# Kernel optimization log

Measured on AMD Instinct MI355X. Metric: run time of the kernel, lower is better.

## Reference

```python
import jax, jax.numpy as jnp
from jax import lax
import numpy as np

NSTART, NOPEN, NHID, NCLOSE, NLAYERS, KSZ, N = 40, 128, 256, 3, 40, 9, 1024
H_STEP = 0.1
PAD = (KSZ - 1) // 2  # 4 -> same-length conv
EPS = 1e-5


def conv1(x, K):
    # x: (1, Cin, N), K: (Cout, Cin, k); cross-correlation like torch F.conv1d
    return lax.conv_general_dilated(x, K, (1,), [(PAD, PAD)],
                                    dimension_numbers=('NCH', 'OIH', 'NCH'))


def conv1T(x, K):
    # torch F.conv_transpose1d(x, K, padding=PAD) == conv1d with swapped-channel,
    # flipped kernel and padding k-1-PAD (= PAD here since k=9, PAD=4)
    Kt = jnp.flip(jnp.swapaxes(K, 0, 1), -1)
    return lax.conv_general_dilated(x, Kt, (1,), [(PAD, PAD)],
                                    dimension_numbers=('NCH', 'OIH', 'NCH'))


def instance_norm(x):
    # x: (1, C, N); normalize per channel over spatial dim, biased var, no affine
    m = jnp.mean(x, axis=-1, keepdims=True)
    v = jnp.var(x, axis=-1, keepdims=True)
    return (x - m) * lax.rsqrt(v + EPS)


def get_graph_lap(Z):
    # Z: (C, N). Normalized Gaussian-affinity graph Laplacian.
    sq = jnp.sum(Z * Z, axis=0)  # (N,)
    D2 = jnp.maximum(sq[:, None] + sq[None, :] - 2.0 * (Z.T @ Z), 0.0)
    sigma = jnp.mean(D2) + 1e-12
    Wg = jnp.exp(-D2 / sigma)
    deg = jnp.sum(Wg, axis=1)
    Dh = lax.rsqrt(deg)
    L = Dh[:, None] * (jnp.diag(deg) - Wg) * Dh[None, :]
    return L, deg


def double_sym_layer(Z, Wi, Bi, L):
    # Z: (nopen, N), Wi: (2, nhid, nopen, 9), Bi: (2, nopen, 1), L: (N, N)
    A0 = instance_norm(conv1((Z + Bi[0])[None], Wi[0]))
    A1 = instance_norm((conv1((Z + Bi[1])[None], Wi[1])[0] @ L)[None])
    A0 = jax.nn.relu(A0)
    A1 = jax.nn.relu(A1)
    A0 = conv1T(A0, Wi[0])[0]
    A1 = conv1T(A1, Wi[1])[0] @ L.T
    return A0 + A1  # (nopen, N)


def setup_inputs() -> dict:
    key = jax.random.key(0)
    k1, k2, k3, k4, k5 = jax.random.split(key, 5)
    Z = jax.random.normal(k1, (NSTART, N), dtype=jnp.float32)
    stdv_o = 0.001 * NOPEN / NSTART
    Kopen = jax.random.uniform(k2, (NOPEN, NSTART), minval=-stdv_o, maxval=stdv_o, dtype=jnp.float32)
    stdv_c = 0.001 * NCLOSE / NOPEN
    Kclose = jax.random.uniform(k3, (NCLOSE, NOPEN), minval=-stdv_c, maxval=stdv_c, dtype=jnp.float32)
    W = jax.random.uniform(k4, (NLAYERS, 2, NHID, NOPEN, KSZ), minval=-1e-4, maxval=1e-4, dtype=jnp.float32)
    Bias = jax.random.uniform(k5, (NLAYERS, 2, NOPEN, 1), dtype=jnp.float32) * 1e-4
    return {"Z": Z, "Kopen": Kopen, "Kclose": Kclose, "W": W, "Bias": Bias}


def reference(Z, Kopen, Kclose, W, Bias):
    h = H_STEP
    Zc = Kopen @ Z          # (nopen, N)
    Zold = Zc
    L, _ = get_graph_lap(Zc)
    for i in range(NLAYERS):
        if i % 10 == 0:
            L, _ = get_graph_lap(Zc)
        Ai = double_sym_layer(Zc, W[i], Bias[i], L)
        Zc, Zold = 2.0 * Zc - Zold - (h * h) * Ai, Zc  # leapfrog step
    return (Kclose @ Zc, Kclose @ Zold)
```

## Files before the change

kernel.cpp:

```cpp
#include <hip/hip_runtime.h>

#define NN 1024
#define NOPEN 128
#define NHID 256
#define NSTART 40
#define NCLOSE 3
#define NLAYERS 40
#define KSZ 9

static constexpr float H2 = 0.01f;
static constexpr float IN_EPS = 1e-5f;

using floatx4 = __attribute__((ext_vector_type(4))) float;
using bfrag = __attribute__((ext_vector_type(8))) short;

__device__ __forceinline__ ushort f2bf(float f) {
    union { float f; unsigned u; } v; v.f = f;
    unsigned r = v.u + 0x7fffu + ((v.u >> 16) & 1u);
    return (ushort)(r >> 16);
}

__device__ __forceinline__ void prepw_piece(const float* __restrict__ W, ushort* __restrict__ Wf1,
                                            ushort* __restrict__ Wf2, int lb, int lsrc, int tid) {
    if (lb < 72) {
        int z = lb / 36, rem = lb % 36;
        int t = rem >> 2, q = rem & 3;
        const float* Wz = W + (size_t)(lsrc * 2 + z) * (NHID * NOPEN * KSZ);
        ushort* dst = Wf1 + (((size_t)(z * 9 + t) * 64 + q * 16) << 9);
#pragma unroll
        for (int r = 0; r < 32; ++r) {
            int ei = r * 256 + tid;
            int g = q * 4 + (ei >> 11);
            int kc = (ei >> 9) & 3;
            int lm = (ei >> 3) & 15, lq = (ei >> 7) & 3;
            int e = ei & 7;
            int co = g * 16 + lm, ci = kc * 32 + lq * 8 + e;
            dst[ei] = f2bf(Wz[co * (NOPEN * KSZ) + ci * KSZ + t]);
        }
    } else {
        int p2 = lb - 72;
        int z = p2 / 36, rem = p2 % 36;
        int t = rem >> 2, q = rem & 3;
        const float* Wz = W + (size_t)(lsrc * 2 + z) * (NHID * NOPEN * KSZ);
        ushort* dst = Wf2 + (((size_t)(z * 9 + t) * 64 + q * 16) << 9);
#pragma unroll
        for (int r = 0; r < 32; ++r) {
            int ei = r * 256 + tid;
            int fb = q * 16 + (ei >> 9);
            int g = fb >> 3, j = fb & 7;
            int lm = (ei >> 3) & 15, lq = (ei >> 7) & 3;
            int e = ei & 7;
            int ci = g * 16 + lm, co = j * 32 + lq * 8 + e;
            dst[ei] = f2bf(Wz[co * (NOPEN * KSZ) + ci * KSZ + t]);
        }
    }
}

__global__ __launch_bounds__(256) void k_open(const float* __restrict__ Kopen, const float* __restrict__ Z,
                       float* __restrict__ Zc, float* __restrict__ Zold,
                       const float* __restrict__ Bias0, ushort* __restrict__ Zct,
                       ushort* __restrict__ At0, ushort* __restrict__ At1,
                       const float* __restrict__ W, ushort* __restrict__ Wf1,
                       ushort* __restrict__ Wf2, float* __restrict__ sig, float* __restrict__ A1) {
    const int v = blockIdx.x, tid = threadIdx.x;
    if (v < 512) {
        int o = v >> 2, n = (v & 3) * 256 + tid;
        float acc = 0.f;
#pragma unroll
        for (int s = 0; s < NSTART; ++s)
            acc = fmaf(Kopen[o * NSTART + s], Z[s * NN + n], acc);
        Zc[o * NN + n] = acc;
        Zold[o * NN + n] = acc;
#pragma unroll
        for (int z = 0; z < 2; ++z)
            Zct[z * (1032 * 128) + (n + 4) * 128 + o] = f2bf(acc + Bias0[z * NOPEN + o]);
    } else if (v < 656) {
        prepw_piece(W, Wf1, Wf2, v - 512, 0, tid);
    } else if (v == 656) {
        if (tid == 0) sig[0] = 0.f;
        for (int idx = tid; idx < 1024; idx += 256) {
            int z = idx >> 9, rr = idx & 511;
            ushort* Zz = Zct + z * (1032 * 128);
            Zz[rr] = 0; Zz[1028 * 128 + rr] = 0;
        }
        for (int idx = tid; idx < 2048; idx += 256) {
            int a = idx >> 10, rr = idx & 1023;
            ushort* A = a ? At1 : At0;
            A[rr] = 0; A[1028 * 256 + rr] = 0;
        }
    } else {
        int b = v - 657;
        size_t base = (size_t)b * 4096 + tid * 4;
        float4 z4 = {0.f, 0.f, 0.f, 0.f};
#pragma unroll
        for (int r = 0; r < 4; ++r) *(float4*)&A1[base + r * 1024] = z4;
    }
}

__global__ __launch_bounds__(256) void k_d2(const float* __restrict__ Zc,
                                            float* __restrict__ D2, float* __restrict__ sig) {
    __shared__ __align__(16) float Zi[32 * 36];
    __shared__ __align__(16) float Zj[32 * 68];
    __shared__ float sqi[32], sqj[64];
    __shared__ float red[4];
    const int tid = threadIdx.x;
    const int tx = tid & 15, ty = tid >> 4;
    const int j0 = blockIdx.x * 64, i0 = blockIdx.y * 32;
    if (tid < 32) sqi[tid] = 0.f;
    else if (tid < 96) sqj[tid - 32] = 0.f;
    float acc[2][4] = {};
    for (int c0 = 0; c0 < NOPEN; c0 += 32) {
        for (int idx = tid; idx < 32 * 32; idx += 256) {
            int c = idx >> 5, ii = idx & 31;
            Zi[c * 36 + ii] = Zc[(c0 + c) * NN + i0 + ii];
        }
        for (int idx = tid; idx < 32 * 64; idx += 256) {
            int c = idx >> 6, jj = idx & 63;
            Zj[c * 68 + jj] = Zc[(c0 + c) * NN + j0 + jj];
        }
        __syncthreads();
        if (tid < 32) {
            float s = 0.f;
            for (int c = 0; c < 32; ++c) { float x = Zi[c * 36 + tid]; s = fmaf(x, x, s); }
            sqi[tid] += s;
        } else if (tid < 96) {
            int jj = tid - 32;
            float s = 0.f;
            for (int c = 0; c < 32; ++c) { float x = Zj[c * 68 + jj]; s = fmaf(x, x, s); }
            sqj[jj] += s;
        }
#pragma unroll 8
        for (int c = 0; c < 32; ++c) {
            float2 zi = *(const float2*)&Zi[c * 36 + ty * 2];
            float4 zj = *(const float4*)&Zj[c * 68 + tx * 4];
            acc[0][0] = fmaf(zi.x, zj.x, acc[0][0]);
            acc[0][1] = fmaf(zi.x, zj.y, acc[0][1]);
            acc[0][2] = fmaf(zi.x, zj.z, acc[0][2]);
            acc[0][3] = fmaf(zi.x, zj.w, acc[0][3]);
            acc[1][0] = fmaf(zi.y, zj.x, acc[1][0]);
            acc[1][1] = fmaf(zi.y, zj.y, acc[1][1]);
            acc[1][2] = fmaf(zi.y, zj.z, acc[1][2]);
            acc[1][3] = fmaf(zi.y, zj.w, acc[1][3]);
        }
        __syncthreads();
    }
    float part = 0.f;
#pragma unroll
    for (int m = 0; m < 2; ++m) {
        int i = i0 + ty * 2 + m;
        float sqi_v = sqi[ty * 2 + m];
        float4 d;
        d.x = fmaxf(sqi_v + sqj[tx * 4 + 0] - 2.f * acc[m][0], 0.f);
        d.y = fmaxf(sqi_v + sqj[tx * 4 + 1] - 2.f * acc[m][1], 0.f);
        d.z = fmaxf(sqi_v + sqj[tx * 4 + 2] - 2.f * acc[m][2], 0.f);
        d.w = fmaxf(sqi_v + sqj[tx * 4 + 3] - 2.f * acc[m][3], 0.f);
        *(float4*)&D2[(size_t)i * NN + j0 + tx * 4] = d;
        part += (d.x + d.y) + (d.z + d.w);
    }
#pragma unroll
    for (int off = 32; off > 0; off >>= 1) part += __shfl_down(part, off);
    if ((tid & 63) == 0) red[tid >> 6] = part;
    __syncthreads();
    if (tid == 0) atomicAdd(sig, red[0] + red[1] + red[2] + red[3]);
}

__global__ void k_deg(const float* __restrict__ D2, const float* __restrict__ sig,
                      float* __restrict__ Dh) {
    __shared__ float red[4];
    int i = blockIdx.x, tid = threadIdx.x;
    float inv = 1.f / (sig[0] * (1.f / 1048576.f) + 1e-12f);
    float4 v = *(const float4*)&D2[(size_t)i * NN + tid * 4];
    float s = __expf(-v.x * inv) + __expf(-v.y * inv) + __expf(-v.z * inv) + __expf(-v.w * inv);
#pragma unroll
    for (int off = 32; off > 0; off >>= 1) s += __shfl_down(s, off);
    if ((tid & 63) == 0) red[tid >> 6] = s;
    __syncthreads();
    if (tid == 0) Dh[i] = rsqrtf(red[0] + red[1] + red[2] + red[3]);
}

__global__ void k_L(const float* __restrict__ D2, const float* __restrict__ sig,
                    const float* __restrict__ Dh, ushort* __restrict__ Lb) {
    int i = blockIdx.x, tid = threadIdx.x;
    int j = tid * 4;
    float inv = 1.f / (sig[0] * (1.f / 1048576.f) + 1e-12f);
    float dhi = Dh[i];
    float4 v = *(const float4*)&D2[(size_t)i * NN + j];
    float4 dj = *(const float4*)&Dh[j];
    float4 o;
    o.x = -dhi * dj.x * __expf(-v.x * inv);
    o.y = -dhi * dj.y * __expf(-v.y * inv);
    o.z = -dhi * dj.z * __expf(-v.z * inv);
    o.w = -dhi * dj.w * __expf(-v.w * inv);
    if (i == j + 0) o.x += 1.f;
    if (i == j + 1) o.y += 1.f;
    if (i == j + 2) o.z += 1.f;
    if (i == j + 3) o.w += 1.f;
    ushort4 ob; ob.x = f2bf(o.x); ob.y = f2bf(o.y); ob.z = f2bf(o.z); ob.w = f2bf(o.w);
    *(ushort4*)&Lb[(size_t)i * NN + j] = ob;
}

__global__ __launch_bounds__(256) void k_convprep(const ushort* __restrict__ Zct,
        const ushort* __restrict__ Wf1, float* __restrict__ C0, ushort* __restrict__ C1b,
        const float* __restrict__ W, ushort* __restrict__ Wf1n, ushort* __restrict__ Wf2n,
        int lnext, int doprep) {
    const int b = blockIdx.x, tid = threadIdx.x;
    if (b >= 512) {
        if (doprep) prepw_piece(W, Wf1n, Wf2n, b - 512, lnext, tid);
        return;
    }
    const int xb = b & 31, yb = (b >> 5) & 7, z = b >> 8;
    const int p0 = xb * 32, co0 = yb * 32;
    __shared__ ushort Xs[40 * 136];
    const ushort* Zz = Zct + z * (1032 * 128);
    for (int idx = tid; idx < 640; idx += 256) {
        int row = idx >> 4, ch = (idx & 15) * 8;
        *(bfrag*)&Xs[row * 136 + ch] = *(const bfrag*)&Zz[(p0 + row) * 128 + ch];
    }
    __syncthreads();
    const int l = tid & 63, wv = tid >> 6;
    const int wm = wv >> 1, wn = wv & 1;
    const int lm = l & 15, lq = l >> 4;
    const ushort* wf = Wf1 + (((size_t)z * 144 + (yb * 2 + wm)) << 11) + l * 8;
    floatx4 acc = {};
    bfrag a_cur[4];
#pragma unroll
    for (int kc = 0; kc < 4; ++kc) a_cur[kc] = *(const bfrag*)(wf + (kc << 9));
    for (int t = 0; t < 9; ++t) {
        bfrag a_nxt[4];
        if (t < 8) {
            const ushort* wptr = wf + (size_t)(t + 1) * (16 << 11);
#pragma unroll
            for (int kc = 0; kc < 4; ++kc) a_nxt[kc] = *(const bfrag*)(wptr + (kc << 9));
        }
        const int xbase = (wn * 16 + lm + t) * 136 + lq * 8;
#pragma unroll
        for (int kc = 0; kc < 4; ++kc) {
            bfrag b0 = *(const bfrag*)&Xs[xbase + kc * 32];
            acc = __builtin_amdgcn_mfma_f32_16x16x32_bf16(a_cur[kc], b0, acc, 0, 0, 0);
        }
#pragma unroll
        for (int kc = 0; kc < 4; ++kc) a_cur[kc] = a_nxt[kc];
    }
    const int cog = co0 + wm * 16 + lq * 4;
    const int pg = p0 + wn * 16 + lm;
#pragma unroll
    for (int r = 0; r < 4; ++r) {
        if (z == 0) C0[(cog + r) * NN + pg] = acc[r];
        else        C1b[(cog + r) * NN + pg] = f2bf(acc[r]);
    }
}

__global__ __launch_bounds__(256) void k_xl_mfma(const ushort* __restrict__ X,
                                                 const ushort* __restrict__ Lb,
                                                 float* __restrict__ Out) {
    __shared__ __align__(16) ushort As[64 * 136];
    __shared__ __align__(16) ushort Bs[64 * 136];
    const int tid = threadIdx.x;
    const int lane = tid & 63, wave = tid >> 6;
    const int wm = wave >> 1, wn = wave & 1;
    const int n0 = blockIdx.x * 64, m0 = blockIdx.y * 64, kc = blockIdx.z * 128;
    {
        int q = tid;
#pragma unroll
        for (int r = 0; r < 4; ++r, q += 256) {
            int row = q >> 4, ch = (q & 15) * 8;
            *(bfrag*)&As[row * 136 + ch] = *(const bfrag*)&X[(m0 + row) * NN + kc + ch];
        }
        q = tid;
#pragma unroll
        for (int r = 0; r < 4; ++r, q += 256) {
            int row = q >> 4, ch = (q & 15) * 8;
            *(bfrag*)&Bs[row * 136 + ch] = *(const bfrag*)&Lb[(n0 + row) * NN + kc + ch];
        }
    }
    __syncthreads();
    floatx4 acc[2][2] = {};
    const int lrow = (lane & 15) * 136;
    const int koff = (lane >> 4) * 8;
#pragma unroll
    for (int ks = 0; ks < 4; ++ks) {
        bfrag a[2], b[2];
#pragma unroll
        for (int i = 0; i < 2; ++i)
            a[i] = *(const bfrag*)&As[(wm * 32 + i * 16) * 136 + lrow + ks * 32 + koff];
#pragma unroll
        for (int j = 0; j < 2; ++j)
            b[j] = *(const bfrag*)&Bs[(wn * 32 + j * 16) * 136 + lrow + ks * 32 + koff];
#pragma unroll
        for (int i = 0; i < 2; ++i)
#pragma unroll
            for (int j = 0; j < 2; ++j)
                acc[i][j] = __builtin_amdgcn_mfma_f32_16x16x32_bf16(a[i], b[j], acc[i][j], 0, 0, 0);
    }
    const int mg0 = m0 + wm * 32 + (lane >> 4) * 4;
    const int ng0 = n0 + wn * 32 + (lane & 15);
#pragma unroll
    for (int i = 0; i < 2; ++i)
#pragma unroll
        for (int j = 0; j < 2; ++j)
#pragma unroll
            for (int r = 0; r < 4; ++r)
                atomicAdd(&Out[(size_t)(mg0 + i * 16 + r) * NN + ng0 + j * 16], acc[i][j][r]);
}

__global__ void k_inorm(const float* __restrict__ C0, const float* __restrict__ A1,
                        float* __restrict__ Mu, float* __restrict__ Rs) {
    const int c = blockIdx.x, arr = blockIdx.y, tid = threadIdx.x;
    __shared__ float rs[4], rq[4];
    const float* in = arr ? A1 : C0;
    float4 v = *(const float4*)&in[c * NN + tid * 4];
    float s = (v.x + v.y) + (v.z + v.w);
    float q = (v.x * v.x + v.y * v.y) + (v.z * v.z + v.w * v.w);
#pragma unroll
    for (int off = 32; off > 0; off >>= 1) { s += __shfl_down(s, off); q += __shfl_down(q, off); }
    if ((tid & 63) == 0) { rs[tid >> 6] = s; rq[tid >> 6] = q; }
    __syncthreads();
    if (tid == 0) {
        float S = rs[0] + rs[1] + rs[2] + rs[3];
        float Q = rq[0] + rq[1] + rq[2] + rq[3];
        float mean = S * (1.f / NN);
        float var = Q * (1.f / NN) - mean * mean;
        Mu[arr * NHID + c] = mean;
        Rs[arr * NHID + c] = rsqrtf(var + IN_EPS);
    }
}

__global__ __launch_bounds__(256) void k_normT(const float* __restrict__ C0,
        const float* __restrict__ A1, const float* __restrict__ Mu, const float* __restrict__ Rs,
        ushort* __restrict__ At0, ushort* __restrict__ At1) {
    const int arr = blockIdx.z;
    const int p0 = blockIdx.x * 32, co0 = blockIdx.y * 64;
    const float* in = arr ? A1 : C0;
    ushort* out = arr ? At1 : At0;
    __shared__ ushort Ls[32 * 72];
    const int tid = threadIdx.x;
#pragma unroll
    for (int r = 0; r < 2; ++r) {
        int idx = r * 256 + tid;
        int col = idx >> 3, pq = idx & 7;
        int co = co0 + col;
        float4 v = *(const float4*)&in[(size_t)co * NN + p0 + pq * 4];
        float m = Mu[arr * NHID + co], sc = Rs[arr * NHID + co];
        Ls[(pq * 4 + 0) * 72 + col] = f2bf(fmaxf((v.x - m) * sc, 0.f));
        Ls[(pq * 4 + 1) * 72 + col] = f2bf(fmaxf((v.y - m) * sc, 0.f));
        Ls[(pq * 4 + 2) * 72 + col] = f2bf(fmaxf((v.z - m) * sc, 0.f));
        Ls[(pq * 4 + 3) * 72 + col] = f2bf(fmaxf((v.w - m) * sc, 0.f));
    }
    __syncthreads();
    {
        int row = tid >> 3, ch = (tid & 7) * 8;
        *(bfrag*)&out[(size_t)(p0 + row + 4) * 256 + co0 + ch] = *(const bfrag*)&Ls[row * 72 + ch];
    }
}

__global__ __launch_bounds__(256) void k_convT_misc(const ushort* __restrict__ At0,
        const ushort* __restrict__ At1, const ushort* __restrict__ Wf2,
        float* __restrict__ Tacc, ushort* __restrict__ T1b,
        float* __restrict__ A1, float* __restrict__ sig) {
    const int b = blockIdx.x, tid = threadIdx.x;
    if (b >= 512) {
        if (b == 576) {
            if (tid == 0) sig[0] = 0.f;
        } else {
            int piece = b - 512;
            size_t base = (size_t)piece * 4096 + tid * 4;
            float4 z4 = {0.f, 0.f, 0.f, 0.f};
#pragma unroll
            for (int r = 0; r < 4; ++r) *(float4*)&A1[base + r * 1024] = z4;
        }
        return;
    }
    const int xb = b & 31, yb = (b >> 5) & 7, z = b >> 8;
    const int p0 = xb * 32, ci0 = yb * 16;
    __shared__ ushort Al[40 * 264];
    __shared__ float Red[2][64][4];
    const ushort* A = z ? At1 : At0;
    for (int idx = tid; idx < 1280; idx += 256) {
        int row = idx >> 5, ch = (idx & 31) * 8;
        *(bfrag*)&Al[row * 264 + ch] = *(const bfrag*)&A[(p0 + row) * 256 + ch];
    }
    __syncthreads();
    const int l = tid & 63, wv = tid >> 6;
    const int ph = wv & 1, kh = wv >> 1;
    const int lm = l & 15, lq = l >> 4;
    const ushort* wbase = Wf2 + (((size_t)z * 72 + yb) << 12) + ((kh * 4) << 9) + l * 8;
    floatx4 acc0 = {}, acc1 = {};
    bfrag a_cur[4];
#pragma unroll
    for (int jj = 0; jj < 4; ++jj) a_cur[jj] = *(const bfrag*)(wbase + (jj << 9));
    for (int t = 0; t < 9; ++t) {
        bfrag a_nxt[4];
        if (t < 8) {
            const ushort* wptr = wbase + (size_t)(t + 1) * (8 << 12);
#pragma unroll
            for (int jj = 0; jj < 4; ++jj) a_nxt[jj] = *(const bfrag*)(wptr + (jj << 9));
        }
        const int abase = (ph * 16 + lm + 8 - t) * 264 + lq * 8;
#pragma unroll
        for (int jj = 0; jj < 4; jj += 2) {
            bfrag b0 = *(const bfrag*)&Al[abase + (kh * 4 + jj) * 32];
            acc0 = __builtin_amdgcn_mfma_f32_16x16x32_bf16(a_cur[jj], b0, acc0, 0, 0, 0);
            bfrag b1 = *(const bfrag*)&Al[abase + (kh * 4 + jj + 1) * 32];
            acc1 = __builtin_amdgcn_mfma_f32_16x16x32_bf16(a_cur[jj + 1], b1, acc1, 0, 0, 0);
        }
#pragma unroll
        for (int jj = 0; jj < 4; ++jj) a_cur[jj] = a_nxt[jj];
    }
    floatx4 acc = acc0 + acc1;
    __syncthreads();
    if (kh == 1) {
#pragma unroll
        for (int r = 0; r < 4; ++r) Red[ph][l][r] = acc[r];
    }
    __syncthreads();
    if (kh == 0) {
#pragma unroll
        for (int r = 0; r < 4; ++r) acc[r] += Red[ph][l][r];
        const int cig = ci0 + lq * 4;
        const int pg = p0 + ph * 16 + lm;
#pragma unroll
        for (int r = 0; r < 4; ++r) {
            if (z == 0) Tacc[(cig + r) * NN + pg] = acc[r];
            else        T1b[(cig + r) * NN + pg] = f2bf(acc[r]);
        }
    }
}

__global__ __launch_bounds__(256) void k_leap(const float* __restrict__ Tacc,
        const float* __restrict__ Zc, float* __restrict__ Zo,
        const float* __restrict__ BiasN, ushort* __restrict__ Zct) {
    const int v = blockIdx.x, tid = threadIdx.x;
    int off = (v * 256 + tid) * 4;
    float4 a = *(const float4*)&Tacc[off];
    float4 zc = *(const float4*)&Zc[off];
    float4 zo = *(const float4*)&Zo[off];
    float4 zn;
    zn.x = 2.f * zc.x - zo.x - H2 * a.x;
    zn.y = 2.f * zc.y - zo.y - H2 * a.y;
    zn.z = 2.f * zc.z - zo.z - H2 * a.z;
    zn.w = 2.f * zc.w - zo.w - H2 * a.w;
    *(float4*)&Zo[off] = zn;
    int ci = off >> 10, n = off & 1023;
#pragma unroll
    for (int z = 0; z < 2; ++z) {
        float bz = BiasN[z * NOPEN + ci];
        ushort* Zz = Zct + z * (1032 * 128);
        Zz[(n + 4) * 128 + ci] = f2bf(zn.x + bz);
        Zz[(n + 5) * 128 + ci] = f2bf(zn.y + bz);
        Zz[(n + 6) * 128 + ci] = f2bf(zn.z + bz);
        Zz[(n + 7) * 128 + ci] = f2bf(zn.w + bz);
    }
}

__global__ void k_close(const float* __restrict__ Kclose, const float* __restrict__ Zc,
                        const float* __restrict__ Zold, float* __restrict__ out) {
    int n = blockIdx.x * 256 + threadIdx.x;
    int o = blockIdx.y;
    const float* Zb = blockIdx.z ? Zold : Zc;
    float a = 0.f;
#pragma unroll
    for (int c = 0; c < NOPEN; ++c) a = fmaf(Kclose[o * NOPEN + c], Zb[c * NN + n], a);
    out[blockIdx.z * (NCLOSE * NN) + o * NN + n] = a;
}

extern "C" void kernel_launch(void* const* d_in, const int* in_sizes, int n_in,
                              void* d_out, int out_size, void* d_ws, size_t ws_size,
                              hipStream_t stream) {
    const float* Z      = (const float*)d_in[0];
    const float* Kopen  = (const float*)d_in[1];
    const float* Kclose = (const float*)d_in[2];
    const float* W      = (const float*)d_in[3];
    const float* Bias   = (const float*)d_in[4];
    float* out = (float*)d_out;
    float* ws  = (float*)d_ws;

    float* Zb0   = ws + 0;
    float* Zb1   = ws + 131072;
    float* D2    = ws + 262144;
    float* C0    = ws + 1310720;
    float* A1    = ws + 1572864;
    float* Tacc  = ws + 1835008;
    float* Dh    = ws + 5111808;
    float* sig   = ws + 5112832;
    float* Mu    = ws + 5113856;
    float* Rs    = ws + 5114880;
    ushort* Lb  = (ushort*)(ws + 5115904);
    ushort* C1b = (ushort*)(ws + 5640192);
    ushort* T1b = (ushort*)(ws + 5771264);
    ushort* Zct = (ushort*)(ws + 5836800);
    ushort* At0 = (ushort*)(ws + 5968896);
    ushort* At1 = (ushort*)(ws + 6100992);
    ushort* Wf1a = (ushort*)(ws + 6233088);
    ushort* Wf2a = (ushort*)(ws + 6380544);
    ushort* Wf1b = (ushort*)(ws + 6528000);
    ushort* Wf2b = (ushort*)(ws + 6675456);

    ushort* Wf1s[2] = { Wf1a, Wf1b };
    ushort* Wf2s[2] = { Wf2a, Wf2b };

    k_open<<<dim3(721), 256, 0, stream>>>(Kopen, Z, Zb0, Zb1, Bias, Zct, At0, At1,
                                          W, Wf1s[0], Wf2s[0], sig, A1);

    float* Zc = Zb0;
    float* Zold = Zb1;
    for (int i = 0; i < NLAYERS; ++i) {
        const int cur = i & 1, nxt = cur ^ 1;
        const int lnext = (i + 1 < NLAYERS) ? i + 1 : NLAYERS - 1;
        const int doprep = (i + 1 < NLAYERS) ? 1 : 0;
        if (i % 10 == 0) {
            k_d2<<<dim3(16, 32), 256, 0, stream>>>(Zc, D2, sig);
            k_deg<<<dim3(NN), 256, 0, stream>>>(D2, sig, Dh);
            k_L<<<dim3(NN), 256, 0, stream>>>(D2, sig, Dh, Lb);
        }
        k_convprep<<<dim3(656), 256, 0, stream>>>(Zct, Wf1s[cur], C0, C1b,
                                                  W, Wf1s[nxt], Wf2s[nxt], lnext, doprep);
        k_xl_mfma<<<dim3(16, 4, 8), 256, 0, stream>>>(C1b, Lb, A1);
        k_inorm<<<dim3(NHID, 2), 256, 0, stream>>>(C0, A1, Mu, Rs);
        k_normT<<<dim3(32, 4, 2), 256, 0, stream>>>(C0, A1, Mu, Rs, At0, At1);
        k_convT_misc<<<dim3(577), 256, 0, stream>>>(At0, At1, Wf2s[cur], Tacc, T1b, A1, sig);
        k_xl_mfma<<<dim3(16, 2, 8), 256, 0, stream>>>(T1b, Lb, Tacc);
        k_leap<<<dim3(128), 256, 0, stream>>>(Tacc, Zc, Zold,
                                              Bias + (size_t)lnext * 2 * NOPEN, Zct);
        float* tmp = Zc; Zc = Zold; Zold = tmp;
    }

    k_close<<<dim3(4, NCLOSE, 2), 256, 0, stream>>>(Kclose, Zc, Zold, out);
}
```

Measured before the change: 1.889 ms.

## Fuse leapfrog update into next layer's conv prep, drop k_leap kernel

Removes the per-layer k_leap kernel by recomputing the leapfrog update on the fly inside k_convprep and k_d2 from Tacc and the previous two states, using a triple-buffered state ring. The conv prep loads fp32 rows, adds bias and converts to bf16 directly into shared memory instead of reading a prebuilt transposed bf16 buffer. Extra blocks in convprep commit the new state and zero A1/sig. This saves one launch per layer and the Zct round trip, but adds redundant strided fp32 loads in the conv staging.

```diff
diff --git a/kernel.cpp b/kernel.cpp
--- a/kernel.cpp
+++ b/kernel.cpp
@@ -18,6 +18,10 @@
     union { float f; unsigned u; } v; v.f = f;
     unsigned r = v.u + 0x7fffu + ((v.u >> 16) & 1u);
     return (ushort)(r >> 16);
+}
+
+__device__ __forceinline__ float leapval(float zc, float zo, float a) {
+    return 2.f * zc - zo - H2 * a;
 }
 
 __device__ __forceinline__ void prepw_piece(const float* __restrict__ W, ushort* __restrict__ Wf1,
@@ -57,8 +61,7 @@
 }
 
 __global__ __launch_bounds__(256) void k_open(const float* __restrict__ Kopen, const float* __restrict__ Z,
-                       float* __restrict__ Zc, float* __restrict__ Zold,
-                       const float* __restrict__ Bias0, ushort* __restrict__ Zct,
+                       float* __restrict__ Z0, float* __restrict__ Z2,
                        ushort* __restrict__ At0, ushort* __restrict__ At1,
                        const float* __restrict__ W, ushort* __restrict__ Wf1,
                        ushort* __restrict__ Wf2, float* __restrict__ sig, float* __restrict__ A1) {
@@ -69,20 +72,12 @@
 #pragma unroll
         for (int s = 0; s < NSTART; ++s)
             acc = fmaf(Kopen[o * NSTART + s], Z[s * NN + n], acc);
-        Zc[o * NN + n] = acc;
-        Zold[o * NN + n] = acc;
-#pragma unroll
-        for (int z = 0; z < 2; ++z)
-            Zct[z * (1032 * 128) + (n + 4) * 128 + o] = f2bf(acc + Bias0[z * NOPEN + o]);
+        Z0[o * NN + n] = acc;
+        Z2[o * NN + n] = acc;
     } else if (v < 656) {
         prepw_piece(W, Wf1, Wf2, v - 512, 0, tid);
     } else if (v == 656) {
         if (tid == 0) sig[0] = 0.f;
-        for (int idx = tid; idx < 1024; idx += 256) {
-            int z = idx >> 9, rr = idx & 511;
-            ushort* Zz = Zct + z * (1032 * 128);
-            Zz[rr] = 0; Zz[1028 * 128 + rr] = 0;
-        }
         for (int idx = tid; idx < 2048; idx += 256) {
             int a = idx >> 10, rr = idx & 1023;
             ushort* A = a ? At1 : At0;
@@ -97,8 +92,9 @@
     }
 }
 
-__global__ __launch_bounds__(256) void k_d2(const float* __restrict__ Zc,
-                                            float* __restrict__ D2, float* __restrict__ sig) {
+__global__ __launch_bounds__(256) void k_d2(const float* __restrict__ Tacc,
+                                            const float* __restrict__ Zm1, const float* __restrict__ Zm2,
+                                            float* __restrict__ D2, float* __restrict__ sig, int fly) {
     __shared__ __align__(16) float Zi[32 * 36];
     __shared__ __align__(16) float Zj[32 * 68];
     __shared__ float sqi[32], sqj[64];
@@ -112,11 +108,15 @@
     for (int c0 = 0; c0 < NOPEN; c0 += 32) {
         for (int idx = tid; idx < 32 * 32; idx += 256) {
             int c = idx >> 5, ii = idx & 31;
-            Zi[c * 36 + ii] = Zc[(c0 + c) * NN + i0 + ii];
+            size_t o = (size_t)(c0 + c) * NN + i0 + ii;
+            float zc = Zm1[o];
+            Zi[c * 36 + ii] = fly ? leapval(zc, Zm2[o], Tacc[o]) : zc;
         }
         for (int idx = tid; idx < 32 * 64; idx += 256) {
             int c = idx >> 6, jj = idx & 63;
-            Zj[c * 68 + jj] = Zc[(c0 + c) * NN + j0 + jj];
+            size_t o = (size_t)(c0 + c) * NN + j0 + jj;
+            float zc = Zm1[o];
+            Zj[c * 68 + jj] = fly ? leapval(zc, Zm2[o], Tacc[o]) : zc;
         }
         __syncthreads();
         if (tid < 32) {
@@ -199,22 +199,62 @@
     *(ushort4*)&Lb[(size_t)i * NN + j] = ob;
 }
 
-__global__ __launch_bounds__(256) void k_convprep(const ushort* __restrict__ Zct,
+__global__ __launch_bounds__(256) void k_convprep(const float* __restrict__ Tacc,
+        const float* __restrict__ Zm1, const float* __restrict__ Zm2, float* __restrict__ Zcommit,
+        const float* __restrict__ BiasI,
         const ushort* __restrict__ Wf1, float* __restrict__ C0, ushort* __restrict__ C1b,
         const float* __restrict__ W, ushort* __restrict__ Wf1n, ushort* __restrict__ Wf2n,
-        int lnext, int doprep) {
+        float* __restrict__ A1, float* __restrict__ sig, int lnext, int doprep, int first) {
     const int b = blockIdx.x, tid = threadIdx.x;
     if (b >= 512) {
-        if (doprep) prepw_piece(W, Wf1n, Wf2n, b - 512, lnext, tid);
+        if (b < 656) {
+            if (doprep) prepw_piece(W, Wf1n, Wf2n, b - 512, lnext, tid);
+        } else if (b < 784) {
+            if (!first) {
+                int b2 = b - 656;
+                int off = (b2 * 256 + tid) * 4;
+                float4 a = *(const float4*)&Tacc[off];
+                float4 zc = *(const float4*)&Zm1[off];
+                float4 zo = *(const float4*)&Zm2[off];
+                float4 zn;
+                zn.x = leapval(zc.x, zo.x, a.x);
+                zn.y = leapval(zc.y, zo.y, a.y);
+                zn.z = leapval(zc.z, zo.z, a.z);
+                zn.w = leapval(zc.w, zo.w, a.w);
+                *(float4*)&Zcommit[off] = zn;
+            }
+        } else if (b < 848) {
+            int piece = b - 784;
+            size_t base = (size_t)piece * 4096 + tid * 4;
+            float4 z4 = {0.f, 0.f, 0.f, 0.f};
+#pragma unroll
+            for (int r = 0; r < 4; ++r) *(float4*)&A1[base + r * 1024] = z4;
+        } else {
+            if (tid == 0) sig[0] = 0.f;
+        }
         return;
     }
     const int xb = b & 31, yb = (b >> 5) & 7, z = b >> 8;
     const int p0 = xb * 32, co0 = yb * 32;
     __shared__ ushort Xs[40 * 136];
-    const ushort* Zz = Zct + z * (1032 * 128);
-    for (int idx = tid; idx < 640; idx += 256) {
-        int row = idx >> 4, ch = (idx & 15) * 8;
-        *(bfrag*)&Xs[row * 136 + ch] = *(const bfrag*)&Zz[(p0 + row) * 128 + ch];
+    {
+        const int ci = tid & 127, nh = tid >> 7;
+        const float bz = BiasI[z * NOPEN + ci];
+        const float* tac = Tacc + (size_t)ci * NN;
+        const float* zc1 = Zm1 + (size_t)ci * NN;
+        const float* zc2 = Zm2 + (size_t)ci * NN;
+#pragma unroll
+        for (int k = 0; k < 20; ++k) {
+            int r = nh * 20 + k;
+            int n = p0 - 4 + r;
+            float x = 0.f;
+            if ((unsigned)n < 1024u) {
+                float zc = zc1[n];
+                float zn = first ? zc : leapval(zc, zc2[n], tac[n]);
+                x = zn + bz;
+            }
+            Xs[r * 136 + ci] = f2bf(x);
+        }
     }
     __syncthreads();
     const int l = tid & 63, wv = tid >> 6;
@@ -353,23 +393,10 @@
     }
 }
 
-__global__ __launch_bounds__(256) void k_convT_misc(const ushort* __restrict__ At0,
+__global__ __launch_bounds__(256) void k_convT(const ushort* __restrict__ At0,
         const ushort* __restrict__ At1, const ushort* __restrict__ Wf2,
-        float* __restrict__ Tacc, ushort* __restrict__ T1b,
-        float* __restrict__ A1, float* __restrict__ sig) {
+        float* __restrict__ Tacc, ushort* __restrict__ T1b) {
     const int b = blockIdx.x, tid = threadIdx.x;
-    if (b >= 512) {
-        if (b == 576) {
-            if (tid == 0) sig[0] = 0.f;
-        } else {
-            int piece = b - 512;
-            size_t base = (size_t)piece * 4096 + tid * 4;
-            float4 z4 = {0.f, 0.f, 0.f, 0.f};
-#pragma unroll
-            for (int r = 0; r < 4; ++r) *(float4*)&A1[base + r * 1024] = z4;
-        }
-        return;
-    }
     const int xb = b & 31, yb = (b >> 5) & 7, z = b >> 8;
     const int p0 = xb * 32, ci0 = yb * 16;
     __shared__ ushort Al[40 * 264];
@@ -426,30 +453,18 @@
     }
 }
 
-__global__ __launch_bounds__(256) void k_leap(const float* __restrict__ Tacc,
-        const float* __restrict__ Zc, float* __restrict__ Zo,
-        const float* __restrict__ BiasN, ushort* __restrict__ Zct) {
-    const int v = blockIdx.x, tid = threadIdx.x;
-    int off = (v * 256 + tid) * 4;
+__global__ __launch_bounds__(256) void k_commit(const float* __restrict__ Tacc,
+        const float* __restrict__ Zm1, const float* __restrict__ Zm2, float* __restrict__ Zout) {
+    const int off = (blockIdx.x * 256 + threadIdx.x) * 4;
     float4 a = *(const float4*)&Tacc[off];
-    float4 zc = *(const float4*)&Zc[off];
-    float4 zo = *(const float4*)&Zo[off];
+    float4 zc = *(const float4*)&Zm1[off];
+    float4 zo = *(const float4*)&Zm2[off];
     float4 zn;
-    zn.x = 2.f * zc.x - zo.x - H2 * a.x;
-    zn.y = 2.f * zc.y - zo.y - H2 * a.y;
-    zn.z = 2.f * zc.z - zo.z - H2 * a.z;
-    zn.w = 2.f * zc.w - zo.w - H2 * a.w;
-    *(float4*)&Zo[off] = zn;
-    int ci = off >> 10, n = off & 1023;
-#pragma unroll
-    for (int z = 0; z < 2; ++z) {
-        float bz = BiasN[z * NOPEN + ci];
-        ushort* Zz = Zct + z * (1032 * 128);
-        Zz[(n + 4) * 128 + ci] = f2bf(zn.x + bz);
-        Zz[(n + 5) * 128 + ci] = f2bf(zn.y + bz);
-        Zz[(n + 6) * 128 + ci] = f2bf(zn.z + bz);
-        Zz[(n + 7) * 128 + ci] = f2bf(zn.w + bz);
-    }
+    zn.x = leapval(zc.x, zo.x, a.x);
+    zn.y = leapval(zc.y, zo.y, a.y);
+    zn.z = leapval(zc.z, zo.z, a.z);
+    zn.w = leapval(zc.w, zo.w, a.w);
+    *(float4*)&Zout[off] = zn;
 }
 
 __global__ void k_close(const float* __restrict__ Kclose, const float* __restrict__ Zc,
@@ -474,12 +489,13 @@
     float* out = (float*)d_out;
     float* ws  = (float*)d_ws;
 
-    float* Zb0   = ws + 0;
-    float* Zb1   = ws + 131072;
+    float* Zr0   = ws + 0;
+    float* Zr1   = ws + 131072;
     float* D2    = ws + 262144;
     float* C0    = ws + 1310720;
     float* A1    = ws + 1572864;
     float* Tacc  = ws + 1835008;
+    float* Zr2   = ws + 1966080;
     float* Dh    = ws + 5111808;
     float* sig   = ws + 5112832;
     float* Mu    = ws + 5113856;
@@ -487,7 +503,6 @@
     ushort* Lb  = (ushort*)(ws + 5115904);
     ushort* C1b = (ushort*)(ws + 5640192);
     ushort* T1b = (ushort*)(ws + 5771264);
-    ushort* Zct = (ushort*)(ws + 5836800);
     ushort* At0 = (ushort*)(ws + 5968896);
     ushort* At1 = (ushort*)(ws + 6100992);
     ushort* Wf1a = (ushort*)(ws + 6233088);
@@ -495,34 +510,38 @@
     ushort* Wf1b = (ushort*)(ws + 6528000);
     ushort* Wf2b = (ushort*)(ws + 6675456);
 
+    float* Zr[3] = { Zr0, Zr1, Zr2 };
     ushort* Wf1s[2] = { Wf1a, Wf1b };
     ushort* Wf2s[2] = { Wf2a, Wf2b };
 
-    k_open<<<dim3(721), 256, 0, stream>>>(Kopen, Z, Zb0, Zb1, Bias, Zct, At0, At1,
+    k_open<<<dim3(721), 256, 0, stream>>>(Kopen, Z, Zr[0], Zr[2], At0, At1,
                                           W, Wf1s[0], Wf2s[0], sig, A1);
 
-    float* Zc = Zb0;
-    float* Zold = Zb1;
     for (int i = 0; i < NLAYERS; ++i) {
         const int cur = i & 1, nxt = cur ^ 1;
         const int lnext = (i + 1 < NLAYERS) ? i + 1 : NLAYERS - 1;
         const int doprep = (i + 1 < NLAYERS) ? 1 : 0;
+        const int first = (i == 0) ? 1 : 0;
+        float* zm1 = Zr[(i + 2) % 3];
+        float* zm2 = Zr[(i + 1) % 3];
+        float* zci = Zr[i % 3];
         if (i % 10 == 0) {
-            k_d2<<<dim3(16, 32), 256, 0, stream>>>(Zc, D2, sig);
+            k_d2<<<dim3(16, 32), 256, 0, stream>>>(Tacc, zm1, zm2, D2, sig, first ? 0 : 1);
             k_deg<<<dim3(NN), 256, 0, stream>>>(D2, sig, Dh);
             k_L<<<dim3(NN), 256, 0, stream>>>(D2, sig, Dh, Lb);
         }
-        k_convprep<<<dim3(656), 256, 0, stream>>>(Zct, Wf1s[cur], C0, C1b,
-                                                  W, Wf1s[nxt], Wf2s[nxt], lnext, doprep);
+        k_convprep<<<dim3(849), 256, 0, stream>>>(Tacc, zm1, zm2, zci,
+                                                  Bias + (size_t)i * 2 * NOPEN,
+                                                  Wf1s[cur], C0, C1b,
+                                                  W, Wf1s[nxt], Wf2s[nxt],
+                                                  A1, sig, lnext, doprep, first);
         k_xl_mfma<<<dim3(16, 4, 8), 256, 0, stream>>>(C1b, Lb, A1);
         k_inorm<<<dim3(NHID, 2), 256, 0, stream>>>(C0, A1, Mu, Rs);
         k_normT<<<dim3(32, 4, 2), 256, 0, stream>>>(C0, A1, Mu, Rs, At0, At1);
-        k_convT_misc<<<dim3(577), 256, 0, stream>>>(At0, At1, Wf2s[cur], Tacc, T1b, A1, sig);
+        k_convT<<<dim3(512), 256, 0, stream>>>(At0, At1, Wf2s[cur], Tacc, T1b);
         k_xl_mfma<<<dim3(16, 2, 8), 256, 0, stream>>>(T1b, Lb, Tacc);
-        k_leap<<<dim3(128), 256, 0, stream>>>(Tacc, Zc, Zold,
-                                              Bias + (size_t)lnext * 2 * NOPEN, Zct);
-        float* tmp = Zc; Zc = Zold; Zold = tmp;
-    }
-
-    k_close<<<dim3(4, NCLOSE, 2), 256, 0, stream>>>(Kclose, Zc, Zold, out);
-}
+    }
+
+    k_commit<<<dim3(128), 256, 0, stream>>>(Tacc, Zr[39 % 3], Zr[38 % 3], Zr[40 % 3]);
+    k_close<<<dim3(4, NCLOSE, 2), 256, 0, stream>>>(Kclose, Zr[40 % 3], Zr[39 % 3], out);
+}
```

Result: slower. 2.723 ms (+44.2%).
